# Kernel tuning notes

Hardware: AMD Instinct MI355X
Metric: run time of the kernel (lower is better)

The kernel has to match this reference:

```python
import jax, jax.numpy as jnp
import numpy as np

D_MODEL = 1024

def setup_inputs() -> dict:
    key = jax.random.key(0)
    ks = jax.random.split(key, 7)
    B, S, D = 4, 2048, D_MODEL
    scale = 1.0 / np.sqrt(D)
    x = jax.random.normal(ks[0], (B, S, D), dtype=jnp.float32)
    Wq = jax.random.normal(ks[1], (D, D), dtype=jnp.float32) * scale
    bq = jnp.zeros((D,), dtype=jnp.float32)
    Wk = jax.random.normal(ks[2], (D, D), dtype=jnp.float32) * scale
    bk = jnp.zeros((D,), dtype=jnp.float32)
    Wv = jax.random.normal(ks[3], (D, D), dtype=jnp.float32) * scale
    bv = jnp.zeros((D,), dtype=jnp.float32)
    return {"x": x, "Wq": Wq, "bq": bq, "Wk": Wk, "bk": bk, "Wv": Wv, "bv": bv}

def reference(x, Wq, bq, Wk, bk, Wv, bv):
    # Single-head attention; scale = 1/sqrt(d_model) as in the torch module (self.d_k = d_model).
    d_k = x.shape[-1]
    q = jnp.einsum('bsd,de->bse', x, Wq) + bq
    k = jnp.einsum('bsd,de->bse', x, Wk) + bk
    v = jnp.einsum('bsd,de->bse', x, Wv) + bv
    scores = jnp.einsum('bqd,bkd->bqk', q, k) / jnp.sqrt(jnp.asarray(d_k, x.dtype))
    attn = jax.nn.softmax(scores, axis=-1)
    return jnp.einsum('bqk,bkd->bqd', attn, v)
```

## Files before the change

kernel.cpp:

```cpp
#include <hip/hip_runtime.h>
#include <hip/hip_bf16.h>

#define DM 1024
#define SEQ 2048
#define NBATCH 4

using f32x4 = __attribute__((ext_vector_type(4))) float;
using s16x8 = __attribute__((ext_vector_type(8))) short;
using u16x4 = __attribute__((ext_vector_type(4))) unsigned short;
using u16x8 = __attribute__((ext_vector_type(8))) unsigned short;

__device__ __forceinline__ unsigned short f2bf(float f) {
  union { float f; unsigned u; } v; v.f = f;
  return (unsigned short)((v.u + 0x7fffu + ((v.u >> 16) & 1u)) >> 16);
}

__global__ void prep_k(const float* __restrict__ X,
                       const float* __restrict__ Wq, const float* __restrict__ Wk,
                       const float* __restrict__ Wv,
                       unsigned short* __restrict__ XB, unsigned short* __restrict__ WT) {
  __shared__ float t[32][33];
  const int b = blockIdx.x;
  if (b < 4096) {
    const int i = b * 256 + threadIdx.x;
    const f32x4* p = (const f32x4*)X;
    f32x4 a = p[2 * i], c = p[2 * i + 1];
    u16x8 o;
#pragma unroll
    for (int q = 0; q < 4; q++) { o[q] = f2bf(a[q]); o[4 + q] = f2bf(c[q]); }
    *(u16x8*)(XB + (size_t)i * 8) = o;
  } else {
    const int r2 = b - 4096;
    const int seg = r2 >> 10;
    const int rem = r2 & 1023;
    const int k0 = (rem >> 5) * 32, n0 = (rem & 31) * 32;
    const float* W = (seg == 0) ? Wq : (seg == 1) ? Wk : Wv;
    unsigned short* out = WT + (size_t)seg * DM * DM;
    const int tr = threadIdx.x >> 5, tc = threadIdx.x & 31;
#pragma unroll
    for (int p = 0; p < 4; p++) {
      int r = tr + p * 8;
      t[r][tc] = W[(size_t)(k0 + r) * DM + n0 + tc];
    }
    __syncthreads();
#pragma unroll
    for (int p = 0; p < 4; p++) {
      int r = tr + p * 8;
      out[(size_t)(n0 + r) * DM + k0 + tc] = f2bf(t[tc][r]);
    }
  }
}

__global__ void combine_k(const float* __restrict__ ms, const float* __restrict__ ss,
                          float* __restrict__ T) {
  const int idx = blockIdx.x * 256 + threadIdx.x;
  const float* m = ms + (size_t)idx * 16;
  const float* s = ss + (size_t)idx * 16;
  float mv[16];
#pragma unroll
  for (int t = 0; t < 16; t++) mv[t] = m[t];
  float M = mv[0];
#pragma unroll
  for (int t = 1; t < 16; t++) M = fmaxf(M, mv[t]);
  float L = 0.f;
#pragma unroll
  for (int t = 0; t < 16; t++) L += s[t] * __expf(mv[t] - M);
  T[idx] = 1.0f;
#pragma unroll
  for (int t = 1; t < 16; t++) T[t * 8192 + idx] = __expf(mv[t - 1] - mv[t]);
  T[16 * 8192 + idx] = __expf(mv[15] - M) / L;
}

template <int MODE, int LDA, int LDB, int KDIM>
__global__ void gemm_nt(const unsigned short* __restrict__ A,
                        const unsigned short* __restrict__ B,
                        void* __restrict__ C0,
                        unsigned short* __restrict__ C1,
                        unsigned short* __restrict__ C2,
                        const float* __restrict__ bq,
                        const float* __restrict__ bk,
                        const float* __restrict__ bv,
                        float* __restrict__ sm,
                        float* __restrict__ sv,
                        const float* __restrict__ Tt) {
  __shared__ unsigned short lbuf[16384];
  __shared__ float redm[256], reds[256];
  unsigned short* lA = lbuf;
  unsigned short* lB = lbuf + 8192;

  const int tid = threadIdx.x;
  const int w = tid >> 6;
  const int L = tid & 63;
  const int wm = w & 1, wn = w >> 1;
  const int qd = L >> 4, ll = L & 15;
  const int bz = blockIdx.z;
  const int tileM = blockIdx.y * 128, tileN = blockIdx.x * 128;

  const unsigned short* Ab = A;
  const unsigned short* Bb = B;
  if (MODE == 1) { Ab += (size_t)bz * SEQ * DM; Bb += (size_t)bz * SEQ * DM; }
  if (MODE == 2) { Ab += (size_t)bz * SEQ * SEQ; Bb += (size_t)bz * DM * SEQ; }

  const int srow = tid >> 3;
  const int pch = tid & 7;
  const int gch = pch ^ (srow & 7);
  const unsigned short* gA = Ab + (size_t)(tileM + srow) * LDA + gch * 8;
  const unsigned short* gB = Bb + (size_t)(tileN + srow) * LDB + gch * 8;
  unsigned short* wA = &lA[srow * 64 + pch * 8];
  unsigned short* wB = &lB[srow * 64 + pch * 8];

  u16x8 rA[4], rB[4];
#define LOADT(kt) do {                                                         \
    const size_t kk_ = (size_t)(kt) * 64;                                      \
    _Pragma("unroll")                                                          \
    for (int i_ = 0; i_ < 4; i_++) {                                           \
      rA[i_] = *(const u16x8*)(gA + (size_t)i_ * 32 * LDA + kk_);              \
      rB[i_] = *(const u16x8*)(gB + (size_t)i_ * 32 * LDB + kk_);              \
    }                                                                          \
  } while (0)
#define WRITET() do {                                                          \
    _Pragma("unroll")                                                          \
    for (int i_ = 0; i_ < 4; i_++) {                                           \
      *(u16x8*)(wA + i_ * 32 * 64) = rA[i_];                                   \
      *(u16x8*)(wB + i_ * 32 * 64) = rB[i_];                                   \
    }                                                                          \
  } while (0)

  f32x4 acc[4][4];
#pragma unroll
  for (int i = 0; i < 4; i++)
#pragma unroll
    for (int j = 0; j < 4; j++) acc[i][j] = (f32x4){0.f, 0.f, 0.f, 0.f};

  const int sw = L & 7;

  float tTn[4][4];
  const float* Tb = nullptr;
  if (MODE == 2) {
    Tb = Tt + (size_t)bz * SEQ + tileM + wm * 64;
#pragma unroll
    for (int i = 0; i < 4; i++)
#pragma unroll
      for (int r = 0; r < 4; r++) tTn[i][r] = Tb[1 * 8192 + i * 16 + qd * 4 + r];
  }

  constexpr int NK = KDIM / 64;
  LOADT(0);
  WRITET();
  __syncthreads();

  for (int k = 0; k < NK; ++k) {
    if (MODE == 2 && k >= 2 && (k & 1) == 0) {
#pragma unroll
      for (int i = 0; i < 4; i++)
#pragma unroll
        for (int j = 0; j < 4; j++)
#pragma unroll
          for (int r = 0; r < 4; r++) acc[i][j][r] *= tTn[i][r];
      const int tn = (k >> 1) + 1;
#pragma unroll
      for (int i = 0; i < 4; i++)
#pragma unroll
        for (int r = 0; r < 4; r++) tTn[i][r] = Tb[(size_t)tn * 8192 + i * 16 + qd * 4 + r];
    }

    if (k + 1 < NK) LOADT(k + 1);

#pragma unroll
    for (int s = 0; s < 2; s++) {
      const int pc = ((s * 4 + qd) ^ sw) * 8;
      s16x8 av[4], bv4[4];
#pragma unroll
      for (int i = 0; i < 4; i++)
        av[i] = *(const s16x8*)&lA[(wm * 64 + i * 16 + ll) * 64 + pc];
#pragma unroll
      for (int j = 0; j < 4; j++)
        bv4[j] = *(const s16x8*)&lB[(wn * 64 + j * 16 + ll) * 64 + pc];
#pragma unroll
      for (int i = 0; i < 4; i++)
#pragma unroll
        for (int j = 0; j < 4; j++)
          acc[i][j] = __builtin_amdgcn_mfma_f32_16x16x32_bf16(av[i], bv4[j], acc[i][j], 0, 0, 0);
    }

    if (k + 1 < NK) {
      __builtin_amdgcn_s_waitcnt(0xC07F);
      __builtin_amdgcn_sched_barrier(0);
      __builtin_amdgcn_s_barrier();
      __builtin_amdgcn_sched_barrier(0);
      WRITET();
      __syncthreads();
    }
  }
#undef LOADT
#undef WRITET

  if (MODE == 0) {
#pragma unroll
    for (int i = 0; i < 4; i++) {
      const int gm0 = tileM + wm * 64 + i * 16 + qd * 4;
#pragma unroll
      for (int j = 0; j < 4; j++) {
        const int gn = tileN + wn * 64 + j * 16 + ll;
        const int seg = gn >> 10;
        const int colin = gn & 1023;
        if (seg == 0) {
          const float bias = bq[colin];
          unsigned short* Q = (unsigned short*)C0;
#pragma unroll
          for (int r = 0; r < 4; r++) Q[(size_t)(gm0 + r) * DM + colin] = f2bf(acc[i][j][r] + bias);
        } else if (seg == 1) {
          const float bias = bk[colin];
#pragma unroll
          for (int r = 0; r < 4; r++) C1[(size_t)(gm0 + r) * DM + colin] = f2bf(acc[i][j][r] + bias);
        } else {
          const float bias = bv[colin];
          u16x4 pk;
#pragma unroll
          for (int r = 0; r < 4; r++) pk[r] = f2bf(acc[i][j][r] + bias);
          const int b = gm0 >> 11, s0 = gm0 & 2047;
          *(u16x4*)(C2 + ((size_t)((b << 10) + colin)) * SEQ + s0) = pk;
        }
      }
    }
  } else if (MODE == 1) {
    __syncthreads();
    float mt[4][4];
#pragma unroll
    for (int i = 0; i < 4; i++)
#pragma unroll
      for (int r = 0; r < 4; r++) {
#pragma unroll
        for (int j = 0; j < 4; j++) acc[i][j][r] *= 0.03125f;
        float v = fmaxf(fmaxf(acc[i][0][r], acc[i][1][r]), fmaxf(acc[i][2][r], acc[i][3][r]));
#pragma unroll
        for (int m = 1; m < 16; m <<= 1) v = fmaxf(v, __shfl_xor(v, m, 16));
        mt[i][r] = v;
      }
    if (ll == 0) {
#pragma unroll
      for (int i = 0; i < 4; i++)
#pragma unroll
        for (int r = 0; r < 4; r++)
          redm[wn * 128 + wm * 64 + i * 16 + qd * 4 + r] = mt[i][r];
    }
    __syncthreads();
#pragma unroll
    for (int i = 0; i < 4; i++)
#pragma unroll
      for (int r = 0; r < 4; r++) {
        const int row = wm * 64 + i * 16 + qd * 4 + r;
        mt[i][r] = fmaxf(redm[row], redm[128 + row]);
      }
#pragma unroll
    for (int i = 0; i < 4; i++)
#pragma unroll
      for (int r = 0; r < 4; r++) {
        const int row = wm * 64 + i * 16 + qd * 4 + r;
        float s = 0.f;
#pragma unroll
        for (int j = 0; j < 4; j++) {
          float e = __expf(acc[i][j][r] - mt[i][r]);
          s += e;
          const int col = wn * 64 + j * 16 + ll;
          lbuf[row * 128 + ((((col >> 4) ^ (row & 7)) << 4) | (col & 15))] = f2bf(e);
        }
#pragma unroll
        for (int m = 1; m < 16; m <<= 1) s += __shfl_xor(s, m, 16);
        if (ll == 0) reds[wn * 128 + row] = s;
      }
    __syncthreads();
    if (wn == 0 && ll == 0) {
#pragma unroll
      for (int i = 0; i < 4; i++)
#pragma unroll
        for (int r = 0; r < 4; r++) {
          const int row = wm * 64 + i * 16 + qd * 4 + r;
          const size_t sidx = ((size_t)bz * SEQ + tileM + row) * 16 + blockIdx.x;
          sm[sidx] = mt[i][r];
          sv[sidx] = reds[row] + reds[128 + row];
        }
    }
    unsigned short* P = (unsigned short*)C0 + (size_t)bz * SEQ * SEQ;
#pragma unroll
    for (int p = 0; p < 8; p++) {
      const int c = p * 256 + tid;
      const int row = c >> 4, cg = c & 15;
      const int phys = ((((cg >> 1) ^ (row & 7)) << 4) | ((cg & 1) << 3));
      u16x8 val = *(const u16x8*)&lbuf[row * 128 + phys];
      *(u16x8*)(P + (size_t)(tileM + row) * SEQ + tileN + cg * 8) = val;
    }
  } else {
    float* O = (float*)C0 + (size_t)bz * SEQ * DM;
#pragma unroll
    for (int i = 0; i < 4; i++) {
      const int gm0 = tileM + wm * 64 + i * 16 + qd * 4;
#pragma unroll
      for (int j = 0; j < 4; j++) {
        const int gn = tileN + wn * 64 + j * 16 + ll;
#pragma unroll
        for (int r = 0; r < 4; r++)
          O[(size_t)(gm0 + r) * DM + gn] = acc[i][j][r] * tTn[i][r];
      }
    }
  }
}

extern "C" void kernel_launch(void* const* d_in, const int* in_sizes, int n_in,
                              void* d_out, int out_size, void* d_ws, size_t ws_size,
                              hipStream_t stream) {
  (void)in_sizes; (void)n_in; (void)out_size; (void)ws_size;
  const float* x  = (const float*)d_in[0];
  const float* Wq = (const float*)d_in[1];
  const float* bq = (const float*)d_in[2];
  const float* Wk = (const float*)d_in[3];
  const float* bk = (const float*)d_in[4];
  const float* Wv = (const float*)d_in[5];
  const float* bv = (const float*)d_in[6];
  float* out = (float*)d_out;
  char* ws = (char*)d_ws;
  unsigned short* xb = (unsigned short*)(ws + 0);
  unsigned short* wt = (unsigned short*)(ws + 16777216);
  unsigned short* qb = (unsigned short*)(ws + 23068672);
  unsigned short* kb = (unsigned short*)(ws + 39845888);
  unsigned short* vt = (unsigned short*)(ws + 56623104);
  unsigned short* P  = (unsigned short*)(ws + 73400320);
  float*          ms = (float*)(ws + 106954752);
  float*          ss = (float*)(ws + 107479040);
  float*          Tt = (float*)(ws + 108003328);

  prep_k<<<7168, 256, 0, stream>>>(x, Wq, Wk, Wv, xb, wt);
  gemm_nt<0, 1024, 1024, 1024><<<dim3(24, 64, 1), 256, 0, stream>>>(
      xb, wt, (void*)qb, kb, vt, bq, bk, bv, nullptr, nullptr, nullptr);
  gemm_nt<1, 1024, 1024, 1024><<<dim3(16, 16, 4), 256, 0, stream>>>(
      qb, kb, (void*)P, nullptr, nullptr, nullptr, nullptr, nullptr, ms, ss, nullptr);
  combine_k<<<32, 256, 0, stream>>>(ms, ss, Tt);
  gemm_nt<2, 2048, 2048, 2048><<<dim3(8, 16, 4), 256, 0, stream>>>(
      P, vt, (void*)out, nullptr, nullptr, nullptr, nullptr, nullptr, nullptr, nullptr, Tt);
}
```

Measured before the change: 276.3 us.

## Remap GEMM tiles onto XCDs for L2 locality and trim softmax-stat LDS reductions

Switches all three GEMM launches to a 1-D grid and decodes block IDs so that blocks landing on the same XCD (bid & 7) work on a contiguous sub-region (a batch half or M/N quadrant). The goal is better per-XCD L2 reuse of the A and B tiles. The score GEMM also drops the separate redm/reds shared arrays: it reuses lbuf for the max reduction and writes per-warp partial row sums straight to global memory. combine_k then adds the two halves, which needs a doubled ss buffer and a moved Tt offset, plus one extra barrier.

```diff
diff --git a/kernel.cpp b/kernel.cpp
--- a/kernel.cpp
+++ b/kernel.cpp
@@ -55,7 +55,7 @@
                           float* __restrict__ T) {
   const int idx = blockIdx.x * 256 + threadIdx.x;
   const float* m = ms + (size_t)idx * 16;
-  const float* s = ss + (size_t)idx * 16;
+  const float* s = ss + (size_t)idx * 32;
   float mv[16];
 #pragma unroll
   for (int t = 0; t < 16; t++) mv[t] = m[t];
@@ -64,7 +64,7 @@
   for (int t = 1; t < 16; t++) M = fmaxf(M, mv[t]);
   float L = 0.f;
 #pragma unroll
-  for (int t = 0; t < 16; t++) L += s[t] * __expf(mv[t] - M);
+  for (int t = 0; t < 16; t++) L += (s[2 * t] + s[2 * t + 1]) * __expf(mv[t] - M);
   T[idx] = 1.0f;
 #pragma unroll
   for (int t = 1; t < 16; t++) T[t * 8192 + idx] = __expf(mv[t - 1] - mv[t]);
@@ -84,7 +84,6 @@
                         float* __restrict__ sv,
                         const float* __restrict__ Tt) {
   __shared__ unsigned short lbuf[16384];
-  __shared__ float redm[256], reds[256];
   unsigned short* lA = lbuf;
   unsigned short* lB = lbuf + 8192;
 
@@ -93,8 +92,25 @@
   const int L = tid & 63;
   const int wm = w & 1, wn = w >> 1;
   const int qd = L >> 4, ll = L & 15;
-  const int bz = blockIdx.z;
-  const int tileM = blockIdx.y * 128, tileN = blockIdx.x * 128;
+
+  const int bid = blockIdx.x;
+  const int xcd = bid & 7, slot = bid >> 3;
+  int bz, tileM, tileN, nT;
+  if (MODE == 0) {
+    const int pm = xcd & 3, pn = xcd >> 2;
+    const int nloc = slot % 12, mloc = slot / 12;
+    bz = 0; tileM = (pm * 16 + mloc) * 128; tileN = (pn * 12 + nloc) * 128; nT = 0;
+  } else if (MODE == 1) {
+    bz = xcd >> 1;
+    const int mh = xcd & 1;
+    const int nloc = slot & 15, mloc = slot >> 4;
+    tileM = (mh * 8 + mloc) * 128; tileN = nloc * 128; nT = nloc;
+  } else {
+    bz = xcd >> 1;
+    const int mh = xcd & 1;
+    const int nloc = slot & 7, mloc = slot >> 3;
+    tileM = (mh * 8 + mloc) * 128; tileN = nloc * 128; nT = nloc;
+  }
 
   const unsigned short* Ab = A;
   const unsigned short* Bb = B;
@@ -237,12 +253,13 @@
         for (int m = 1; m < 16; m <<= 1) v = fmaxf(v, __shfl_xor(v, m, 16));
         mt[i][r] = v;
       }
+    float* fred = (float*)lbuf;
     if (ll == 0) {
 #pragma unroll
       for (int i = 0; i < 4; i++)
 #pragma unroll
         for (int r = 0; r < 4; r++)
-          redm[wn * 128 + wm * 64 + i * 16 + qd * 4 + r] = mt[i][r];
+          fred[wn * 128 + wm * 64 + i * 16 + qd * 4 + r] = mt[i][r];
     }
     __syncthreads();
 #pragma unroll
@@ -250,8 +267,9 @@
 #pragma unroll
       for (int r = 0; r < 4; r++) {
         const int row = wm * 64 + i * 16 + qd * 4 + r;
-        mt[i][r] = fmaxf(redm[row], redm[128 + row]);
-      }
+        mt[i][r] = fmaxf(fred[row], fred[128 + row]);
+      }
+    __syncthreads();
 #pragma unroll
     for (int i = 0; i < 4; i++)
 #pragma unroll
@@ -267,20 +285,13 @@
         }
 #pragma unroll
         for (int m = 1; m < 16; m <<= 1) s += __shfl_xor(s, m, 16);
-        if (ll == 0) reds[wn * 128 + row] = s;
-      }
-    __syncthreads();
-    if (wn == 0 && ll == 0) {
-#pragma unroll
-      for (int i = 0; i < 4; i++)
-#pragma unroll
-        for (int r = 0; r < 4; r++) {
-          const int row = wm * 64 + i * 16 + qd * 4 + r;
-          const size_t sidx = ((size_t)bz * SEQ + tileM + row) * 16 + blockIdx.x;
-          sm[sidx] = mt[i][r];
-          sv[sidx] = reds[row] + reds[128 + row];
+        if (ll == 0) {
+          const size_t base = (size_t)bz * SEQ + tileM + row;
+          sv[base * 32 + nT * 2 + wn] = s;
+          if (wn == 0) sm[base * 16 + nT] = mt[i][r];
         }
-    }
+      }
+    __syncthreads();
     unsigned short* P = (unsigned short*)C0 + (size_t)bz * SEQ * SEQ;
 #pragma unroll
     for (int p = 0; p < 8; p++) {
@@ -327,14 +338,14 @@
   unsigned short* P  = (unsigned short*)(ws + 73400320);
   float*          ms = (float*)(ws + 106954752);
   float*          ss = (float*)(ws + 107479040);
-  float*          Tt = (float*)(ws + 108003328);
+  float*          Tt = (float*)(ws + 108527616);
 
   prep_k<<<7168, 256, 0, stream>>>(x, Wq, Wk, Wv, xb, wt);
-  gemm_nt<0, 1024, 1024, 1024><<<dim3(24, 64, 1), 256, 0, stream>>>(
+  gemm_nt<0, 1024, 1024, 1024><<<1536, 256, 0, stream>>>(
       xb, wt, (void*)qb, kb, vt, bq, bk, bv, nullptr, nullptr, nullptr);
-  gemm_nt<1, 1024, 1024, 1024><<<dim3(16, 16, 4), 256, 0, stream>>>(
+  gemm_nt<1, 1024, 1024, 1024><<<1024, 256, 0, stream>>>(
       qb, kb, (void*)P, nullptr, nullptr, nullptr, nullptr, nullptr, ms, ss, nullptr);
   combine_k<<<32, 256, 0, stream>>>(ms, ss, Tt);
-  gemm_nt<2, 2048, 2048, 2048><<<dim3(8, 16, 4), 256, 0, stream>>>(
+  gemm_nt<2, 2048, 2048, 2048><<<512, 256, 0, stream>>>(
       P, vt, (void*)out, nullptr, nullptr, nullptr, nullptr, nullptr, nullptr, nullptr, Tt);
 }
```

Result: no change. 273.1 us (-1.2%).
